# Kernel optimization log

Measured on AMD Instinct MI355X. Metric: run time of the kernel, lower is better.

Reference implementation:

```python
import jax, jax.numpy as jnp
import numpy as np

LINHAS, COLUNAS, DIM, BATCH = 32, 32, 256, 2048
NEURONS = LINHAS * COLUNAS
TAXA_INICIAL = 0.5
SIGMA_INICIAL = max(LINHAS, COLUNAS) / 2.0  # 16.0


def _grid_locs():
    # matches tf.meshgrid default 'xy' indexing, stacked then flattened
    x = jnp.arange(LINHAS, dtype=jnp.float32)
    y = jnp.arange(COLUNAS, dtype=jnp.float32)
    g = jnp.stack(jnp.meshgrid(x, y), axis=-1)  # (COLUNAS, LINHAS, 2)
    return g.reshape(-1, 2)


def setup_inputs() -> dict:
    key = jax.random.key(0)
    k1, k2 = jax.random.split(key)
    X = jax.random.normal(k1, (BATCH, DIM), dtype=jnp.float32)
    # keras 'random_normal' initializer: stddev 0.05
    pesos = jax.random.normal(k2, (NEURONS, DIM), dtype=jnp.float32) * 0.05
    return {
        "X": X,
        "pesos": pesos,
        "localizacoes": _grid_locs(),
        "passo_atual": 100,
        "total_passos": 1000,
    }


def reference(X, pesos, localizacoes, passo_atual, total_passos):
    frac = jnp.float32(passo_atual) / jnp.float32(total_passos)
    taxa = TAXA_INICIAL * jnp.exp(-frac)
    sigma = SIGMA_INICIAL * jnp.exp(-frac)

    # squared-euclidean distances (B, N)
    x2 = jnp.sum(X * X, axis=1, keepdims=True)
    w2 = jnp.sum(pesos * pesos, axis=1)
    dist = x2 + w2 - 2.0 * (X @ pesos.T)

    bmu_idx = jnp.argmin(dist, axis=1)            # (B,)
    bmu_loc = localizacoes[bmu_idx]               # (B, 2)

    # grid distances and Gaussian neighborhood (B, N)
    dist_grade = jnp.sum((localizacoes[None, :, :] - bmu_loc[:, None, :]) ** 2, axis=2)
    h = jnp.exp(-dist_grade / (2.0 * sigma ** 2))

    # delta_total = mean_b taxa * h[b,n] * (X[b,d] - W[n,d]), computed without
    # materializing the (B, N, D) tensor:
    B = jnp.float32(X.shape[0])
    delta_total = taxa * (jnp.einsum('bn,bd->nd', h, X) - jnp.sum(h, axis=0)[:, None] * pesos) / B

    new_pesos = pesos + delta_total
    return new_pesos
```

## Files before the change

### kernel.cpp

```cpp
#include <hip/hip_runtime.h>
#include <float.h>

#define Bsz 2048
#define Nn  1024
#define Dd  256

typedef __attribute__((ext_vector_type(8))) short bf16x8;
typedef __attribute__((ext_vector_type(4))) float f32x4;
typedef unsigned long long u64;

union b8u4 { bf16x8 v; uint4 u; };

__device__ __forceinline__ unsigned short bfr(float x) {
    unsigned u = __float_as_uint(x);
    u += 0x7fffu + ((u >> 16) & 1u);
    return (unsigned short)(u >> 16);
}

__device__ __forceinline__ void som_params(const int* __restrict__ step,
                                           const int* __restrict__ total,
                                           float* taxa, float* inv2s2) {
    float frac = (float)(*step) / (float)(*total);
    float e = __expf(-frac);
    *taxa = 0.5f * e;
    float sigma = 16.0f * e;
    *inv2s2 = 1.0f / (2.0f * sigma * sigma);
}

__device__ __forceinline__ u64 packsc(float f, int n) {
    unsigned u = __float_as_uint(f);
    u = (u & 0x80000000u) ? ~u : (u | 0x80000000u);
    return ((u64)u << 32) | (unsigned)n;
}

__device__ __forceinline__ float split8t(const float* __restrict__ src,
                                         bf16x8* hi, bf16x8* lo) {
    float4 v0 = *(const float4*)src;
    float4 v1 = *(const float4*)(src + 4);
    float f[8] = {v0.x, v0.y, v0.z, v0.w, v1.x, v1.y, v1.z, v1.w};
    float s = 0.f;
    unsigned hp[4], lp[4];
    #pragma unroll
    for (int p = 0; p < 4; ++p) {
        float a = f[2*p], b = f[2*p+1];
        unsigned ua = __float_as_uint(a), ub = __float_as_uint(b);
        unsigned ha = ua & 0xffff0000u, hb = ub & 0xffff0000u;
        float la = a - __uint_as_float(ha);
        float lb = b - __uint_as_float(hb);
        hp[p] = (ua >> 16) | hb;
        lp[p] = (__float_as_uint(la) >> 16) | (__float_as_uint(lb) & 0xffff0000u);
        s = fmaf(a, a, s); s = fmaf(b, b, s);
    }
    b8u4 H, L;
    H.u = make_uint4(hp[0], hp[1], hp[2], hp[3]);
    L.u = make_uint4(lp[0], lp[1], lp[2], lp[3]);
    *hi = H.v; *lo = L.v;
    return s;
}

__global__ __launch_bounds__(256) void fused_pre(
    const float* __restrict__ X, const float* __restrict__ W,
    ushort* __restrict__ Xt, u64* __restrict__ ppack)
{
    __shared__ float ld[64][33];
    __shared__ u64 lmin[2][2][64];

    const int t = threadIdx.x, bid = blockIdx.x;
    const int w = t >> 6, l = t & 63;
    const int lr = l & 15, lg = l >> 4;

    {
        const int wm = w & 1, wn = w >> 1;
        const int b0 = (bid >> 4) * 128 + wm * 64;
        const int n0 = (bid & 15) * 64 + wn * 32;

        f32x4 acc[4][2];
        #pragma unroll
        for (int m = 0; m < 4; ++m)
            #pragma unroll
            for (int n = 0; n < 2; ++n) { f32x4 z = {0.f,0.f,0.f,0.f}; acc[m][n] = z; }
        float w2a[2] = {0.f, 0.f};

        #pragma unroll 2
        for (int kd = 0; kd < Dd; kd += 32) {
            bf16x8 ah[4], al[4], bh[2], bl[2];
            #pragma unroll
            for (int m = 0; m < 4; ++m)
                split8t(&X[(size_t)(b0 + m*16 + lr) * Dd + kd + lg*8], &ah[m], &al[m]);
            #pragma unroll
            for (int nf = 0; nf < 2; ++nf)
                w2a[nf] += split8t(&W[(size_t)(n0 + nf*16 + lr) * Dd + kd + lg*8],
                                   &bh[nf], &bl[nf]);
            #pragma unroll
            for (int m = 0; m < 4; ++m)
                #pragma unroll
                for (int nf = 0; nf < 2; ++nf) {
                    acc[m][nf] = __builtin_amdgcn_mfma_f32_16x16x32_bf16(ah[m], bh[nf], acc[m][nf], 0, 0, 0);
                    acc[m][nf] = __builtin_amdgcn_mfma_f32_16x16x32_bf16(ah[m], bl[nf], acc[m][nf], 0, 0, 0);
                    acc[m][nf] = __builtin_amdgcn_mfma_f32_16x16x32_bf16(al[m], bh[nf], acc[m][nf], 0, 0, 0);
                }
        }

        #pragma unroll
        for (int nf = 0; nf < 2; ++nf) {
            w2a[nf] += __shfl_xor(w2a[nf], 16, 64);
            w2a[nf] += __shfl_xor(w2a[nf], 32, 64);
        }
        const int ni0 = n0 + lr, ni1 = n0 + 16 + lr;

        #pragma unroll
        for (int m = 0; m < 4; ++m)
            #pragma unroll
            for (int r = 0; r < 4; ++r) {
                u64 p0 = packsc(w2a[0] - 2.f * acc[m][0][r], ni0);
                u64 p1 = packsc(w2a[1] - 2.f * acc[m][1][r], ni1);
                u64 pm = p1 < p0 ? p1 : p0;
                #pragma unroll
                for (int msk = 1; msk < 16; msk <<= 1) {
                    unsigned plo = (unsigned)pm, phi = (unsigned)(pm >> 32);
                    plo = __shfl_xor(plo, msk, 64);
                    phi = __shfl_xor(phi, msk, 64);
                    u64 o = ((u64)phi << 32) | plo;
                    if (o < pm) pm = o;
                }
                if (lr == 0) lmin[wm][wn][m*16 + lg*4 + r] = pm;
            }
        __syncthreads();
        if (t < 128) {
            const int bwm = t >> 6, bb = t & 63;
            u64 a = lmin[bwm][0][bb], c = lmin[bwm][1][bb];
            u64 pm = c < a ? c : a;
            const int b = (bid >> 4) * 128 + bwm * 64 + bb;
            ppack[(size_t)(bid & 15) * Bsz + b] = pm;
        }
    }

    {
        const int b0t = (bid & 31) * 64;
        const int d0t = (bid >> 5) * 32;

        #pragma unroll
        for (int p = 0; p < 2; ++p) {
            int flat = p * 256 + t;
            int row = flat >> 3, c4 = flat & 7;
            float4 v = *(const float4*)&X[(size_t)(b0t + row) * Dd + d0t + c4 * 4];
            ld[row][c4*4+0] = v.x; ld[row][c4*4+1] = v.y;
            ld[row][c4*4+2] = v.z; ld[row][c4*4+3] = v.w;
        }
        __syncthreads();
        const int d  = t >> 3;
        const int bs = (t & 7) * 8;
        bf16x8 o;
        #pragma unroll
        for (int j = 0; j < 8; ++j) o[j] = (short)bfr(ld[bs + j][d]);
        *(bf16x8*)&Xt[(size_t)(d0t + d) * Bsz + b0t + bs] = o;
    }
}

__global__ __launch_bounds__(1024, 4) void acc_finish(
    const ushort* __restrict__ Xt, const u64* __restrict__ ppack,
    const float* __restrict__ W, const int* __restrict__ step,
    const int* __restrict__ total, float* __restrict__ out)
{
    __shared__ float red[8][32][36];
    __shared__ float hws[16][32];
    __shared__ ushort bidx[Bsz];

    const int t = threadIdx.x, w = t >> 6, l = t & 63;
    const int lr = l & 15, lg = l >> 4;
    const int n0 = blockIdx.x * 32;
    const int d0 = blockIdx.y * 32;

    #pragma unroll
    for (int q = 0; q < 2; ++q) {
        const int b = q * 1024 + t;
        u64 pm = ppack[b];
        #pragma unroll
        for (int g = 1; g < 16; ++g) {
            u64 c = ppack[(size_t)g * Bsz + b];
            if (c < pm) pm = c;
        }
        bidx[b] = (ushort)(pm & 0xffffu);
    }
    __syncthreads();

    float taxa, inv2s2;
    som_params(step, total, &taxa, &inv2s2);

    const float fny  = (float)(n0 >> 5);
    const float fnx0 = (float)lr;
    const float fnx1 = (float)(lr + 16);

    f32x4 acc[2][2];
    #pragma unroll
    for (int m = 0; m < 2; ++m)
        #pragma unroll
        for (int nf = 0; nf < 2; ++nf) { f32x4 z = {0.f,0.f,0.f,0.f}; acc[m][nf] = z; }
    float hs0 = 0.f, hs1 = 0.f;

    #pragma unroll
    for (int ks = 0; ks < 4; ++ks) {
        const int bk = w * 128 + ks * 32 + lg * 8;
        bf16x8 am0, am1;
        #pragma unroll
        for (int j = 0; j < 8; ++j) {
            unsigned idx = bidx[bk + j];
            float bx = (float)(idx & 31), by = (float)(idx >> 5);
            float dy  = fny - by;
            float dy2 = dy * dy;
            float dx0 = fnx0 - bx, dx1 = fnx1 - bx;
            float h0 = __expf(-(dx0*dx0 + dy2) * inv2s2);
            float h1 = __expf(-(dx1*dx1 + dy2) * inv2s2);
            am0[j] = (short)bfr(h0);
            am1[j] = (short)bfr(h1);
            hs0 += h0; hs1 += h1;
        }
        bf16x8 bx0 = *(const bf16x8*)&Xt[(size_t)(d0 + lr)      * Bsz + bk];
        bf16x8 bx1 = *(const bf16x8*)&Xt[(size_t)(d0 + 16 + lr) * Bsz + bk];
        acc[0][0] = __builtin_amdgcn_mfma_f32_16x16x32_bf16(am0, bx0, acc[0][0], 0, 0, 0);
        acc[0][1] = __builtin_amdgcn_mfma_f32_16x16x32_bf16(am0, bx1, acc[0][1], 0, 0, 0);
        acc[1][0] = __builtin_amdgcn_mfma_f32_16x16x32_bf16(am1, bx0, acc[1][0], 0, 0, 0);
        acc[1][1] = __builtin_amdgcn_mfma_f32_16x16x32_bf16(am1, bx1, acc[1][1], 0, 0, 0);
    }

    hs0 += __shfl_xor(hs0, 16, 64); hs0 += __shfl_xor(hs0, 32, 64);
    hs1 += __shfl_xor(hs1, 16, 64); hs1 += __shfl_xor(hs1, 32, 64);
    if (l < 16) { hws[w][l] = hs0; hws[w][16 + l] = hs1; }

    if (w < 8) {
        #pragma unroll
        for (int m = 0; m < 2; ++m)
            #pragma unroll
            for (int nf = 0; nf < 2; ++nf)
                #pragma unroll
                for (int r = 0; r < 4; ++r)
                    red[w][m*16 + lg*4 + r][nf*16 + lr] = acc[m][nf][r];
    }
    __syncthreads();
    if (w >= 8) {
        #pragma unroll
        for (int m = 0; m < 2; ++m)
            #pragma unroll
            for (int nf = 0; nf < 2; ++nf)
                #pragma unroll
                for (int r = 0; r < 4; ++r)
                    red[w - 8][m*16 + lg*4 + r][nf*16 + lr] += acc[m][nf][r];
    }
    __syncthreads();

    const float invB = 1.0f / 2048.0f;
    const int nl = t >> 5;
    const int dl = t & 31;
    float s = 0.f, hsn = 0.f;
    #pragma unroll
    for (int ww = 0; ww < 8; ++ww) s += red[ww][nl][dl];
    #pragma unroll
    for (int ww = 0; ww < 16; ++ww) hsn += hws[ww][nl];
    const int n = n0 + nl;
    const int d = d0 + dl;
    const float wv = W[(size_t)n * Dd + d];
    out[(size_t)n * Dd + d] = wv + taxa * (s - hsn * wv) * invB;
}

extern "C" void kernel_launch(void* const* d_in, const int* in_sizes, int n_in,
                              void* d_out, int out_size, void* d_ws, size_t ws_size,
                              hipStream_t stream)
{
    const float* X    = (const float*)d_in[0];
    const float* W    = (const float*)d_in[1];
    const int* step   = (const int*)d_in[3];
    const int* total  = (const int*)d_in[4];
    float* out = (float*)d_out;

    char* p = (char*)d_ws;
    ushort* Xt    = (ushort*)p; p += 1048576;
    u64*    ppack = (u64*)p;    p += 262144;

    fused_pre <<<256, 256, 0, stream>>>(X, W, Xt, ppack);
    acc_finish<<<dim3(32, 8), 1024, 0, stream>>>(Xt, ppack, W, step, total, out);
}
```

Measured before the change: 36.65 us.

## Replace neighborhood GEMM with BMU scatter and separable Gaussian convolution

```diff
diff --git a/kernel.cpp b/kernel.cpp
--- a/kernel.cpp
+++ b/kernel.cpp
@@ -10,12 +10,6 @@
 typedef unsigned long long u64;
 
 union b8u4 { bf16x8 v; uint4 u; };
-
-__device__ __forceinline__ unsigned short bfr(float x) {
-    unsigned u = __float_as_uint(x);
-    u += 0x7fffu + ((u >> 16) & 1u);
-    return (unsigned short)(u >> 16);
-}
 
 __device__ __forceinline__ void som_params(const int* __restrict__ step,
                                            const int* __restrict__ total,
@@ -58,208 +52,221 @@
     return s;
 }
 
-__global__ __launch_bounds__(256) void fused_pre(
+__global__ __launch_bounds__(256) void bmu_pre(
     const float* __restrict__ X, const float* __restrict__ W,
-    ushort* __restrict__ Xt, u64* __restrict__ ppack)
-{
-    __shared__ float ld[64][33];
+    u64* __restrict__ ppack)
+{
     __shared__ u64 lmin[2][2][64];
 
     const int t = threadIdx.x, bid = blockIdx.x;
     const int w = t >> 6, l = t & 63;
     const int lr = l & 15, lg = l >> 4;
 
-    {
-        const int wm = w & 1, wn = w >> 1;
-        const int b0 = (bid >> 4) * 128 + wm * 64;
-        const int n0 = (bid & 15) * 64 + wn * 32;
-
-        f32x4 acc[4][2];
+    const int wm = w & 1, wn = w >> 1;
+    const int b0 = (bid >> 4) * 128 + wm * 64;
+    const int n0 = (bid & 15) * 64 + wn * 32;
+
+    f32x4 acc[4][2];
+    #pragma unroll
+    for (int m = 0; m < 4; ++m)
+        #pragma unroll
+        for (int n = 0; n < 2; ++n) { f32x4 z = {0.f,0.f,0.f,0.f}; acc[m][n] = z; }
+    float w2a[2] = {0.f, 0.f};
+
+    #pragma unroll 2
+    for (int kd = 0; kd < Dd; kd += 32) {
+        bf16x8 ah[4], al[4], bh[2], bl[2];
         #pragma unroll
         for (int m = 0; m < 4; ++m)
-            #pragma unroll
-            for (int n = 0; n < 2; ++n) { f32x4 z = {0.f,0.f,0.f,0.f}; acc[m][n] = z; }
-        float w2a[2] = {0.f, 0.f};
-
-        #pragma unroll 2
-        for (int kd = 0; kd < Dd; kd += 32) {
-            bf16x8 ah[4], al[4], bh[2], bl[2];
-            #pragma unroll
-            for (int m = 0; m < 4; ++m)
-                split8t(&X[(size_t)(b0 + m*16 + lr) * Dd + kd + lg*8], &ah[m], &al[m]);
-            #pragma unroll
-            for (int nf = 0; nf < 2; ++nf)
-                w2a[nf] += split8t(&W[(size_t)(n0 + nf*16 + lr) * Dd + kd + lg*8],
-                                   &bh[nf], &bl[nf]);
-            #pragma unroll
-            for (int m = 0; m < 4; ++m)
-                #pragma unroll
-                for (int nf = 0; nf < 2; ++nf) {
-                    acc[m][nf] = __builtin_amdgcn_mfma_f32_16x16x32_bf16(ah[m], bh[nf], acc[m][nf], 0, 0, 0);
-                    acc[m][nf] = __builtin_amdgcn_mfma_f32_16x16x32_bf16(ah[m], bl[nf], acc[m][nf], 0, 0, 0);
-                    acc[m][nf] = __builtin_amdgcn_mfma_f32_16x16x32_bf16(al[m], bh[nf], acc[m][nf], 0, 0, 0);
-                }
-        }
-
-        #pragma unroll
-        for (int nf = 0; nf < 2; ++nf) {
-            w2a[nf] += __shfl_xor(w2a[nf], 16, 64);
-            w2a[nf] += __shfl_xor(w2a[nf], 32, 64);
-        }
-        const int ni0 = n0 + lr, ni1 = n0 + 16 + lr;
-
+            split8t(&X[(size_t)(b0 + m*16 + lr) * Dd + kd + lg*8], &ah[m], &al[m]);
+        #pragma unroll
+        for (int nf = 0; nf < 2; ++nf)
+            w2a[nf] += split8t(&W[(size_t)(n0 + nf*16 + lr) * Dd + kd + lg*8],
+                               &bh[nf], &bl[nf]);
         #pragma unroll
         for (int m = 0; m < 4; ++m)
             #pragma unroll
-            for (int r = 0; r < 4; ++r) {
-                u64 p0 = packsc(w2a[0] - 2.f * acc[m][0][r], ni0);
-                u64 p1 = packsc(w2a[1] - 2.f * acc[m][1][r], ni1);
-                u64 pm = p1 < p0 ? p1 : p0;
-                #pragma unroll
-                for (int msk = 1; msk < 16; msk <<= 1) {
-                    unsigned plo = (unsigned)pm, phi = (unsigned)(pm >> 32);
-                    plo = __shfl_xor(plo, msk, 64);
-                    phi = __shfl_xor(phi, msk, 64);
-                    u64 o = ((u64)phi << 32) | plo;
-                    if (o < pm) pm = o;
-                }
-                if (lr == 0) lmin[wm][wn][m*16 + lg*4 + r] = pm;
+            for (int nf = 0; nf < 2; ++nf) {
+                acc[m][nf] = __builtin_amdgcn_mfma_f32_16x16x32_bf16(ah[m], bh[nf], acc[m][nf], 0, 0, 0);
+                acc[m][nf] = __builtin_amdgcn_mfma_f32_16x16x32_bf16(ah[m], bl[nf], acc[m][nf], 0, 0, 0);
+                acc[m][nf] = __builtin_amdgcn_mfma_f32_16x16x32_bf16(al[m], bh[nf], acc[m][nf], 0, 0, 0);
             }
-        __syncthreads();
-        if (t < 128) {
-            const int bwm = t >> 6, bb = t & 63;
-            u64 a = lmin[bwm][0][bb], c = lmin[bwm][1][bb];
-            u64 pm = c < a ? c : a;
-            const int b = (bid >> 4) * 128 + bwm * 64 + bb;
-            ppack[(size_t)(bid & 15) * Bsz + b] = pm;
-        }
-    }
-
-    {
-        const int b0t = (bid & 31) * 64;
-        const int d0t = (bid >> 5) * 32;
-
-        #pragma unroll
-        for (int p = 0; p < 2; ++p) {
-            int flat = p * 256 + t;
-            int row = flat >> 3, c4 = flat & 7;
-            float4 v = *(const float4*)&X[(size_t)(b0t + row) * Dd + d0t + c4 * 4];
-            ld[row][c4*4+0] = v.x; ld[row][c4*4+1] = v.y;
-            ld[row][c4*4+2] = v.z; ld[row][c4*4+3] = v.w;
-        }
-        __syncthreads();
-        const int d  = t >> 3;
-        const int bs = (t & 7) * 8;
-        bf16x8 o;
-        #pragma unroll
-        for (int j = 0; j < 8; ++j) o[j] = (short)bfr(ld[bs + j][d]);
-        *(bf16x8*)&Xt[(size_t)(d0t + d) * Bsz + b0t + bs] = o;
-    }
-}
-
-__global__ __launch_bounds__(1024, 4) void acc_finish(
-    const ushort* __restrict__ Xt, const u64* __restrict__ ppack,
-    const float* __restrict__ W, const int* __restrict__ step,
-    const int* __restrict__ total, float* __restrict__ out)
-{
-    __shared__ float red[8][32][36];
-    __shared__ float hws[16][32];
-    __shared__ ushort bidx[Bsz];
-
-    const int t = threadIdx.x, w = t >> 6, l = t & 63;
-    const int lr = l & 15, lg = l >> 4;
-    const int n0 = blockIdx.x * 32;
-    const int d0 = blockIdx.y * 32;
-
-    #pragma unroll
-    for (int q = 0; q < 2; ++q) {
-        const int b = q * 1024 + t;
+    }
+
+    #pragma unroll
+    for (int nf = 0; nf < 2; ++nf) {
+        w2a[nf] += __shfl_xor(w2a[nf], 16, 64);
+        w2a[nf] += __shfl_xor(w2a[nf], 32, 64);
+    }
+    const int ni0 = n0 + lr, ni1 = n0 + 16 + lr;
+
+    #pragma unroll
+    for (int m = 0; m < 4; ++m)
+        #pragma unroll
+        for (int r = 0; r < 4; ++r) {
+            u64 p0 = packsc(w2a[0] - 2.f * acc[m][0][r], ni0);
+            u64 p1 = packsc(w2a[1] - 2.f * acc[m][1][r], ni1);
+            u64 pm = p1 < p0 ? p1 : p0;
+            #pragma unroll
+            for (int msk = 1; msk < 16; msk <<= 1) {
+                unsigned plo = (unsigned)pm, phi = (unsigned)(pm >> 32);
+                plo = __shfl_xor(plo, msk, 64);
+                phi = __shfl_xor(phi, msk, 64);
+                u64 o = ((u64)phi << 32) | plo;
+                if (o < pm) pm = o;
+            }
+            if (lr == 0) lmin[wm][wn][m*16 + lg*4 + r] = pm;
+        }
+    __syncthreads();
+    if (t < 128) {
+        const int bwm = t >> 6, bb = t & 63;
+        u64 a = lmin[bwm][0][bb], c = lmin[bwm][1][bb];
+        u64 pm = c < a ? c : a;
+        const int b = (bid >> 4) * 128 + bwm * 64 + bb;
+        ppack[(size_t)(bid & 15) * Bsz + b] = pm;
+    }
+}
+
+__global__ __launch_bounds__(256) void scatter_t(
+    const float* __restrict__ X, const u64* __restrict__ ppack,
+    const int* __restrict__ step, const int* __restrict__ total,
+    float* __restrict__ T, int* __restrict__ cnt_g)
+{
+    __shared__ float  S_l[Nn][8];
+    __shared__ float  Ex_l[32][32];
+    __shared__ ushort bidx_l[Bsz];
+    __shared__ int    cnt_l[Nn];
+
+    const int t = threadIdx.x, bid = blockIdx.x;
+    const int d0 = bid * 8;
+
+    float taxa, inv2s2;
+    som_params(step, total, &taxa, &inv2s2);
+
+    #pragma unroll
+    for (int i = 0; i < 32; ++i) ((float*)S_l)[t + 256*i] = 0.f;
+    #pragma unroll
+    for (int i = 0; i < 4; ++i) cnt_l[t + 256*i] = 0;
+    #pragma unroll
+    for (int i = 0; i < 4; ++i) {
+        int idx = t + 256*i;
+        int nx = idx >> 5, gx = idx & 31;
+        float d = (float)(nx - gx);
+        Ex_l[nx][gx] = __expf(-(d*d) * inv2s2);
+    }
+    __syncthreads();
+
+    #pragma unroll
+    for (int i = 0; i < 8; ++i) {
+        const int b = t + 256*i;
         u64 pm = ppack[b];
         #pragma unroll
         for (int g = 1; g < 16; ++g) {
             u64 c = ppack[(size_t)g * Bsz + b];
             if (c < pm) pm = c;
         }
-        bidx[b] = (ushort)(pm & 0xffffu);
-    }
-    __syncthreads();
+        ushort gi = (ushort)(pm & 0xffffu);
+        bidx_l[b] = gi;
+        atomicAdd(&cnt_l[gi], 1);
+    }
+    __syncthreads();
+
+    if (bid == 0) {
+        #pragma unroll
+        for (int i = 0; i < 4; ++i) cnt_g[t + 256*i] = cnt_l[t + 256*i];
+    }
+
+    {
+        const int dt = t & 7, bg = t >> 3;
+        #pragma unroll 8
+        for (int i = 0; i < 64; ++i) {
+            const int b = bg * 64 + i;
+            const int g = bidx_l[b];
+            atomicAdd(&S_l[g][dt], X[(size_t)b * Dd + d0 + dt]);
+        }
+    }
+    __syncthreads();
+
+    {
+        const int gyg = t >> 5;
+        const int nxc = (t >> 3) & 3;
+        const int dt  = t & 7;
+        #pragma unroll
+        for (int gyl = 0; gyl < 4; ++gyl) {
+            const int gy = gyg * 4 + gyl;
+            float a8[8] = {0,0,0,0,0,0,0,0};
+            #pragma unroll
+            for (int gx = 0; gx < 32; ++gx) {
+                float s = S_l[gy*32 + gx][dt];
+                #pragma unroll
+                for (int j = 0; j < 8; ++j)
+                    a8[j] = fmaf(Ex_l[nxc*8 + j][gx], s, a8[j]);
+            }
+            #pragma unroll
+            for (int j = 0; j < 8; ++j)
+                T[(size_t)(gy*32 + nxc*8 + j) * Dd + d0 + dt] = a8[j];
+        }
+    }
+}
+
+__global__ __launch_bounds__(256) void finish(
+    const float* __restrict__ T, const int* __restrict__ cnt_g,
+    const float* __restrict__ W, const int* __restrict__ step,
+    const int* __restrict__ total, float* __restrict__ out)
+{
+    __shared__ float Exc_l[4][32];
+    __shared__ float hsum_l[4];
+
+    const int t = threadIdx.x, bid = blockIdx.x;
+    const int n0 = bid * 4;
+    const int ny = n0 >> 5;
+    const int nxb = n0 & 31;
 
     float taxa, inv2s2;
     som_params(step, total, &taxa, &inv2s2);
-
-    const float fny  = (float)(n0 >> 5);
-    const float fnx0 = (float)lr;
-    const float fnx1 = (float)(lr + 16);
-
-    f32x4 acc[2][2];
-    #pragma unroll
-    for (int m = 0; m < 2; ++m)
-        #pragma unroll
-        for (int nf = 0; nf < 2; ++nf) { f32x4 z = {0.f,0.f,0.f,0.f}; acc[m][nf] = z; }
-    float hs0 = 0.f, hs1 = 0.f;
-
-    #pragma unroll
-    for (int ks = 0; ks < 4; ++ks) {
-        const int bk = w * 128 + ks * 32 + lg * 8;
-        bf16x8 am0, am1;
-        #pragma unroll
-        for (int j = 0; j < 8; ++j) {
-            unsigned idx = bidx[bk + j];
-            float bx = (float)(idx & 31), by = (float)(idx >> 5);
-            float dy  = fny - by;
-            float dy2 = dy * dy;
-            float dx0 = fnx0 - bx, dx1 = fnx1 - bx;
-            float h0 = __expf(-(dx0*dx0 + dy2) * inv2s2);
-            float h1 = __expf(-(dx1*dx1 + dy2) * inv2s2);
-            am0[j] = (short)bfr(h0);
-            am1[j] = (short)bfr(h1);
-            hs0 += h0; hs1 += h1;
-        }
-        bf16x8 bx0 = *(const bf16x8*)&Xt[(size_t)(d0 + lr)      * Bsz + bk];
-        bf16x8 bx1 = *(const bf16x8*)&Xt[(size_t)(d0 + 16 + lr) * Bsz + bk];
-        acc[0][0] = __builtin_amdgcn_mfma_f32_16x16x32_bf16(am0, bx0, acc[0][0], 0, 0, 0);
-        acc[0][1] = __builtin_amdgcn_mfma_f32_16x16x32_bf16(am0, bx1, acc[0][1], 0, 0, 0);
-        acc[1][0] = __builtin_amdgcn_mfma_f32_16x16x32_bf16(am1, bx0, acc[1][0], 0, 0, 0);
-        acc[1][1] = __builtin_amdgcn_mfma_f32_16x16x32_bf16(am1, bx1, acc[1][1], 0, 0, 0);
-    }
-
-    hs0 += __shfl_xor(hs0, 16, 64); hs0 += __shfl_xor(hs0, 32, 64);
-    hs1 += __shfl_xor(hs1, 16, 64); hs1 += __shfl_xor(hs1, 32, 64);
-    if (l < 16) { hws[w][l] = hs0; hws[w][16 + l] = hs1; }
-
-    if (w < 8) {
-        #pragma unroll
-        for (int m = 0; m < 2; ++m)
-            #pragma unroll
-            for (int nf = 0; nf < 2; ++nf)
-                #pragma unroll
-                for (int r = 0; r < 4; ++r)
-                    red[w][m*16 + lg*4 + r][nf*16 + lr] = acc[m][nf][r];
-    }
-    __syncthreads();
-    if (w >= 8) {
-        #pragma unroll
-        for (int m = 0; m < 2; ++m)
-            #pragma unroll
-            for (int nf = 0; nf < 2; ++nf)
-                #pragma unroll
-                for (int r = 0; r < 4; ++r)
-                    red[w - 8][m*16 + lg*4 + r][nf*16 + lr] += acc[m][nf][r];
-    }
-    __syncthreads();
-
     const float invB = 1.0f / 2048.0f;
-    const int nl = t >> 5;
-    const int dl = t & 31;
-    float s = 0.f, hsn = 0.f;
-    #pragma unroll
-    for (int ww = 0; ww < 8; ++ww) s += red[ww][nl][dl];
-    #pragma unroll
-    for (int ww = 0; ww < 16; ++ww) hsn += hws[ww][nl];
-    const int n = n0 + nl;
-    const int d = d0 + dl;
-    const float wv = W[(size_t)n * Dd + d];
-    out[(size_t)n * Dd + d] = wv + taxa * (s - hsn * wv) * invB;
+
+    if (t < 128) {
+        const int nxl = t >> 5, gy = t & 31;
+        const int nx = nxb + nxl;
+        float s = 0.f;
+        #pragma unroll
+        for (int gx = 0; gx < 32; ++gx) {
+            float d = (float)(nx - gx);
+            s = fmaf(__expf(-(d*d) * inv2s2), (float)cnt_g[gy*32 + gx], s);
+        }
+        Exc_l[nxl][gy] = s;
+    }
+    __syncthreads();
+    if (t < 4) {
+        float s = 0.f;
+        #pragma unroll
+        for (int gy = 0; gy < 32; ++gy) {
+            float d = (float)(ny - gy);
+            s = fmaf(__expf(-(d*d) * inv2s2), Exc_l[t][gy], s);
+        }
+        hsum_l[t] = s;
+    }
+    __syncthreads();
+
+    float ey[32];
+    #pragma unroll
+    for (int gy = 0; gy < 32; ++gy) {
+        float d = (float)(ny - gy);
+        ey[gy] = __expf(-(d*d) * inv2s2);
+    }
+
+    #pragma unroll
+    for (int nl = 0; nl < 4; ++nl) {
+        const int n = n0 + nl;
+        const int nx = nxb + nl;
+        float acc = 0.f;
+        #pragma unroll
+        for (int gy = 0; gy < 32; ++gy)
+            acc = fmaf(ey[gy], T[(size_t)(gy*32 + nx) * Dd + t], acc);
+        const float wv = W[(size_t)n * Dd + t];
+        out[(size_t)n * Dd + t] = wv + taxa * (acc - hsum_l[nl] * wv) * invB;
+    }
 }
 
 extern "C" void kernel_launch(void* const* d_in, const int* in_sizes, int n_in,
@@ -273,9 +280,11 @@
     float* out = (float*)d_out;
 
     char* p = (char*)d_ws;
-    ushort* Xt    = (ushort*)p; p += 1048576;
-    u64*    ppack = (u64*)p;    p += 262144;
-
-    fused_pre <<<256, 256, 0, stream>>>(X, W, Xt, ppack);
-    acc_finish<<<dim3(32, 8), 1024, 0, stream>>>(Xt, ppack, W, step, total, out);
-}
+    u64*   ppack = (u64*)p;   p += 262144;
+    float* T     = (float*)p; p += 1048576;
+    int*   cnt   = (int*)p;   p += 4096;
+
+    bmu_pre  <<<256, 256, 0, stream>>>(X, W, ppack);
+    scatter_t<<<32, 256, 0, stream>>>(X, ppack, step, total, T, cnt);
+    finish   <<<256, 256, 0, stream>>>(T, cnt, W, step, total, out);
+}
```

After: 73.06 us. +99.3%, slower.
